# Kernel tuning notes

Hardware: AMD Instinct MI355X
Metric: run time of the kernel (lower is better)

Reference implementation:

```python
import jax, jax.numpy as jnp
import numpy as np

SHIFT = 10  # matches init kwarg shift=10


def _best_shift(x, y):
    """Per-sample argmax-Pearson shift. x, y: [B, T] -> s_best: [B] int.

    For shift s, the original pairs (x[i], y[i+s]) for all valid i
    (sf<0: x[-sf:], y[:sf]; sf>0: x[:-sf], y[sf:]).
    We realize this with a clipped gather + validity mask and compute a
    masked Pearson correlation for all 2*SHIFT+1 shifts at once.
    """
    B, T = x.shape
    shifts = jnp.arange(-SHIFT, SHIFT + 1)               # [S]
    idx = jnp.arange(T)[None, :] + shifts[:, None]        # [S, T]
    valid = (idx >= 0) & (idx < T)                        # [S, T]
    idx_c = jnp.clip(idx, 0, T - 1)
    ys = y[:, idx_c]                                      # [B, S, T] shifted y
    v = valid[None].astype(x.dtype)                       # [1, S, T]
    n = v.sum(-1)                                         # [1, S] = T - |s|
    mx = (x[:, None, :] * v).sum(-1) / n                  # [B, S]
    my = (ys * v).sum(-1) / n                             # [B, S]
    dx = (x[:, None, :] - mx[..., None]) * v              # centered, masked
    dy = (ys - my[..., None]) * v
    cov = (dx * dy).sum(-1)
    corr = cov / jnp.sqrt((dx * dx).sum(-1) * (dy * dy).sum(-1))  # [B, S]
    return shifts[jnp.argmax(corr, axis=-1)]              # [B] (first max, like torch)


def _masked_mse(x, y, s_best):
    """fn = MSE (mean reduction) over the best-shift overlap, per sample."""
    B, T = x.shape
    idx = jnp.arange(T)[None, :] + s_best[:, None]        # [B, T]
    valid = (idx >= 0) & (idx < T)
    yb = jnp.take_along_axis(y, jnp.clip(idx, 0, T - 1), axis=1)
    vf = valid.astype(x.dtype)
    d = (x - yb) * vf
    return (d * d).sum(-1) / vf.sum(-1)                   # [B]


def setup_inputs() -> dict:
    key = jax.random.key(0)
    k1, k2 = jax.random.split(key)
    B, T = 2048, 4096
    x = jax.random.normal(k1, (B, T), dtype=jnp.float32)
    # make y a noisy shifted copy of x so the shift search is meaningful
    y = jnp.roll(x, 3, axis=1) + 0.1 * jax.random.normal(k2, (B, T), dtype=jnp.float32)
    return {"x": x, "y": y}


def reference(x, y):
    s_best = _best_shift(x, y)             # [B], int (no grad path)
    return jnp.mean(_masked_mse(x, y, s_best))
```

## Files before the change

kernel.cpp:

```cpp
#include <hip/hip_runtime.h>

#define TLEN 4096
#define NQ (TLEN / 4)
#define NSHIFT 21
#define SHIFT 10
#define NTHR 256

__global__ __launch_bounds__(NTHR, 4)
void shift_corr_kernel(const float* __restrict__ x, const float* __restrict__ y,
                       float* __restrict__ mse_out)
{
    __shared__ float redbuf[4][32];

    const int tid  = threadIdx.x;
    const int row  = blockIdx.x;
    const int lane = tid & 63;
    const int wid  = tid >> 6;

    const float* xrow = x + (size_t)row * TLEN;
    const float* yrow = y + (size_t)row * TLEN;
    const float4* xg = (const float4*)xrow;
    const float4* yq = (const float4*)yrow;

    float4 xq[4];
    #pragma unroll
    for (int it = 0; it < 4; ++it)
        xq[it] = xg[tid + it * NTHR];

    float sxy[NSHIFT];
    #pragma unroll
    for (int k = 0; k < NSHIFT; ++k) sxy[k] = 0.f;
    float sx = 0.f, sxx = 0.f, sy = 0.f, syy = 0.f;

    #pragma unroll
    for (int it = 0; it < 4; ++it) {
        const int c = tid + it * NTHR;
        float xv[4] = {xq[it].x, xq[it].y, xq[it].z, xq[it].w};
        float yw[28];
        #pragma unroll
        for (int k = 0; k < 7; ++k) {
            int qi = c + k - 3;
            int qc = qi < 0 ? 0 : (qi > NQ - 1 ? NQ - 1 : qi);
            float msk = (qi == qc) ? 1.f : 0.f;
            float4 v = yq[qc];
            yw[4*k+0] = v.x * msk; yw[4*k+1] = v.y * msk;
            yw[4*k+2] = v.z * msk; yw[4*k+3] = v.w * msk;
        }
        #pragma unroll
        for (int l = 0; l < 4; ++l) {
            float xl = xv[l];
            sx += xl; sxx = fmaf(xl, xl, sxx);
            float yl = yw[12 + l];
            sy += yl; syy = fmaf(yl, yl, syy);
            #pragma unroll
            for (int si = 0; si < NSHIFT; ++si)
                sxy[si] = fmaf(xl, yw[l + si + 2], sxy[si]);
        }
    }

    float vals[32];
    #pragma unroll
    for (int k = 0; k < NSHIFT; ++k) vals[k] = sxy[k];
    vals[21] = sx; vals[22] = sxx; vals[23] = sy; vals[24] = syy;
    #pragma unroll
    for (int k = NSHIFT + 4; k < 32; ++k) vals[k] = 0.f;

    #pragma unroll
    for (int b = 5; b >= 1; --b) {
        const int mask = 1 << b;
        const int half = 1 << (b - 1);
        const bool keepLow = ((lane >> b) & 1) == 0;
        #pragma unroll
        for (int j = 0; j < half; ++j) {
            float send = keepLow ? vals[j + half] : vals[j];
            float recv = __shfl_xor(send, mask, 64);
            vals[j] = (keepLow ? vals[j] : vals[j + half]) + recv;
        }
    }
    {
        float recv = __shfl_xor(vals[0], 1, 64);
        float tot = vals[0] + recv;
        if ((lane & 1) == 0) redbuf[wid][(lane >> 1) & 31] = tot;
    }
    __syncthreads();

    if (wid == 0) {
        const int v = lane & 31;
        float S = redbuf[0][v] + redbuf[1][v] + redbuf[2][v] + redbuf[3][v];
        float Sx  = __shfl(S, 21, 64);
        float Sxx = __shfl(S, 22, 64);
        float Sy  = __shfl(S, 23, 64);
        float Syy = __shfl(S, 24, 64);

        float corr = -1e30f, mse = 0.f;
        int bsi = lane;
        if (lane < NSHIFT) {
            const int s = lane - SHIFT;
            const int k = s < 0 ? -s : s;
            float ax = 0.f, axx = 0.f, ay = 0.f, ayy = 0.f;
            if (s >= 0) {
                for (int j = 0; j < k; ++j) {
                    float xv = xrow[TLEN - 1 - j];
                    float yv = yrow[j];
                    ax += xv; axx = fmaf(xv, xv, axx);
                    ay += yv; ayy = fmaf(yv, yv, ayy);
                }
            } else {
                for (int j = 0; j < k; ++j) {
                    float xv = xrow[j];
                    float yv = yrow[TLEN - 1 - j];
                    ax += xv; axx = fmaf(xv, xv, axx);
                    ay += yv; ayy = fmaf(yv, yv, ayy);
                }
            }
            const float n = (float)(TLEN - k);
            float Sxs = Sx - ax, Sxxs = Sxx - axx;
            float Sys = Sy - ay, Syys = Syy - ayy;
            float Sxys = S;
            float cov = Sxys - Sxs * Sys / n;
            float vx  = Sxxs - Sxs * Sxs / n;
            float vy  = Syys - Sys * Sys / n;
            corr = cov * rsqrtf(vx * vy);
            mse  = (Sxxs + Syys - 2.f * Sxys) / n;
        }
        #pragma unroll
        for (int m = 32; m >= 1; m >>= 1) {
            float oc = __shfl_xor(corr, m, 64);
            float om = __shfl_xor(mse,  m, 64);
            int  osi = __shfl_xor(bsi,  m, 64);
            if (oc > corr || (oc == corr && osi < bsi)) {
                corr = oc; mse = om; bsi = osi;
            }
        }
        if (lane == 0) mse_out[row] = mse;
    }
}

__global__ __launch_bounds__(NTHR)
void finalize_kernel(const float* __restrict__ mse, float* __restrict__ out, int B)
{
    __shared__ float red[4];
    int tid = threadIdx.x;
    int lane = tid & 63, wid = tid >> 6;
    const float4* m4 = (const float4*)mse;
    float a = 0.f;
    for (int i = tid; i < B / 4; i += NTHR) {
        float4 v = m4[i];
        a += (v.x + v.y) + (v.z + v.w);
    }
    #pragma unroll
    for (int off = 32; off > 0; off >>= 1)
        a += __shfl_down(a, off, 64);
    if (lane == 0) red[wid] = a;
    __syncthreads();
    if (tid == 0) out[0] = (red[0] + red[1] + red[2] + red[3]) / (float)B;
}

extern "C" void kernel_launch(void* const* d_in, const int* in_sizes, int n_in,
                              void* d_out, int out_size, void* d_ws, size_t ws_size,
                              hipStream_t stream)
{
    const float* x = (const float*)d_in[0];
    const float* y = (const float*)d_in[1];
    float* out = (float*)d_out;
    float* ws  = (float*)d_ws;
    const int B = in_sizes[0] / TLEN;

    shift_corr_kernel<<<B, NTHR, 0, stream>>>(x, y, ws);
    finalize_kernel<<<1, NTHR, 0, stream>>>(ws, out, B);
}
```

Before: 96.36 us.

## Split each row across four blocks and add a separate Pearson kernel

The single per-row kernel is split in two. The first kernel launches four blocks per row, each processing one quarter of the row, and writes partial sums for 21 shifts plus the x and y moments to the workspace. A second kernel of one wave per row combines the partials, applies the edge corrections and selects the best shift. This raises grid parallelism and lowers per-thread registers, at the cost of an extra kernel launch, a workspace round trip, and re-reading the y halo at quarter boundaries.

```diff
diff --git a/kernel.cpp b/kernel.cpp
--- a/kernel.cpp
+++ b/kernel.cpp
@@ -5,27 +5,38 @@
 #define NSHIFT 21
 #define SHIFT 10
 #define NTHR 256
+#define PARTS 4
+#define NVAL 32
 
 __global__ __launch_bounds__(NTHR, 4)
-void shift_corr_kernel(const float* __restrict__ x, const float* __restrict__ y,
-                       float* __restrict__ mse_out)
+void partial_kernel(const float* __restrict__ x, const float* __restrict__ y,
+                    float* __restrict__ partial)
 {
-    __shared__ float redbuf[4][32];
+    __shared__ float redbuf[4][NVAL];
 
     const int tid  = threadIdx.x;
-    const int row  = blockIdx.x;
+    const int row  = blockIdx.x >> 2;
+    const int part = blockIdx.x & 3;
     const int lane = tid & 63;
     const int wid  = tid >> 6;
 
-    const float* xrow = x + (size_t)row * TLEN;
-    const float* yrow = y + (size_t)row * TLEN;
-    const float4* xg = (const float4*)xrow;
-    const float4* yq = (const float4*)yrow;
+    const float4* xg = (const float4*)(x + (size_t)row * TLEN);
+    const float4* yq = (const float4*)(y + (size_t)row * TLEN);
+    const int c = part * NTHR + tid;
 
-    float4 xq[4];
+    float4 xv4 = xg[c];
+    float xv[4] = {xv4.x, xv4.y, xv4.z, xv4.w};
+
+    float yw[28];
     #pragma unroll
-    for (int it = 0; it < 4; ++it)
-        xq[it] = xg[tid + it * NTHR];
+    for (int k = 0; k < 7; ++k) {
+        int qi = c + k - 3;
+        int qc = qi < 0 ? 0 : (qi > NQ - 1 ? NQ - 1 : qi);
+        float msk = (qi == qc) ? 1.f : 0.f;
+        float4 v = yq[qc];
+        yw[4*k+0] = v.x * msk; yw[4*k+1] = v.y * msk;
+        yw[4*k+2] = v.z * msk; yw[4*k+3] = v.w * msk;
+    }
 
     float sxy[NSHIFT];
     #pragma unroll
@@ -33,29 +44,14 @@
     float sx = 0.f, sxx = 0.f, sy = 0.f, syy = 0.f;
 
     #pragma unroll
-    for (int it = 0; it < 4; ++it) {
-        const int c = tid + it * NTHR;
-        float xv[4] = {xq[it].x, xq[it].y, xq[it].z, xq[it].w};
-        float yw[28];
+    for (int l = 0; l < 4; ++l) {
+        float xl = xv[l];
+        sx += xl; sxx = fmaf(xl, xl, sxx);
+        float yl = yw[12 + l];
+        sy += yl; syy = fmaf(yl, yl, syy);
         #pragma unroll
-        for (int k = 0; k < 7; ++k) {
-            int qi = c + k - 3;
-            int qc = qi < 0 ? 0 : (qi > NQ - 1 ? NQ - 1 : qi);
-            float msk = (qi == qc) ? 1.f : 0.f;
-            float4 v = yq[qc];
-            yw[4*k+0] = v.x * msk; yw[4*k+1] = v.y * msk;
-            yw[4*k+2] = v.z * msk; yw[4*k+3] = v.w * msk;
-        }
-        #pragma unroll
-        for (int l = 0; l < 4; ++l) {
-            float xl = xv[l];
-            sx += xl; sxx = fmaf(xl, xl, sxx);
-            float yl = yw[12 + l];
-            sy += yl; syy = fmaf(yl, yl, syy);
-            #pragma unroll
-            for (int si = 0; si < NSHIFT; ++si)
-                sxy[si] = fmaf(xl, yw[l + si + 2], sxy[si]);
-        }
+        for (int si = 0; si < NSHIFT; ++si)
+            sxy[si] = fmaf(xl, yw[l + si + 2], sxy[si]);
     }
 
     float vals[32];
@@ -84,56 +80,74 @@
     }
     __syncthreads();
 
-    if (wid == 0) {
-        const int v = lane & 31;
-        float S = redbuf[0][v] + redbuf[1][v] + redbuf[2][v] + redbuf[3][v];
-        float Sx  = __shfl(S, 21, 64);
-        float Sxx = __shfl(S, 22, 64);
-        float Sy  = __shfl(S, 23, 64);
-        float Syy = __shfl(S, 24, 64);
+    if (wid == 0 && lane < 32) {
+        float S = redbuf[0][lane] + redbuf[1][lane] + redbuf[2][lane] + redbuf[3][lane];
+        partial[(size_t)blockIdx.x * NVAL + lane] = S;
+    }
+}
 
-        float corr = -1e30f, mse = 0.f;
-        int bsi = lane;
-        if (lane < NSHIFT) {
-            const int s = lane - SHIFT;
-            const int k = s < 0 ? -s : s;
-            float ax = 0.f, axx = 0.f, ay = 0.f, ayy = 0.f;
-            if (s >= 0) {
-                for (int j = 0; j < k; ++j) {
-                    float xv = xrow[TLEN - 1 - j];
-                    float yv = yrow[j];
-                    ax += xv; axx = fmaf(xv, xv, axx);
-                    ay += yv; ayy = fmaf(yv, yv, ayy);
-                }
-            } else {
-                for (int j = 0; j < k; ++j) {
-                    float xv = xrow[j];
-                    float yv = yrow[TLEN - 1 - j];
-                    ax += xv; axx = fmaf(xv, xv, axx);
-                    ay += yv; ayy = fmaf(yv, yv, ayy);
-                }
+__global__ __launch_bounds__(64)
+void pearson_kernel(const float* __restrict__ x, const float* __restrict__ y,
+                    const float* __restrict__ partial, float* __restrict__ mse_out)
+{
+    const int row  = blockIdx.x;
+    const int lane = threadIdx.x;
+    const int v = lane & 31;
+
+    const float* xrow = x + (size_t)row * TLEN;
+    const float* yrow = y + (size_t)row * TLEN;
+
+    float S = 0.f;
+    #pragma unroll
+    for (int p = 0; p < PARTS; ++p)
+        S += partial[(size_t)(row * PARTS + p) * NVAL + v];
+
+    float Sx  = __shfl(S, 21, 64);
+    float Sxx = __shfl(S, 22, 64);
+    float Sy  = __shfl(S, 23, 64);
+    float Syy = __shfl(S, 24, 64);
+
+    float corr = -1e30f, mse = 0.f;
+    int bsi = lane;
+    if (lane < NSHIFT) {
+        const int s = lane - SHIFT;
+        const int k = s < 0 ? -s : s;
+        float ax = 0.f, axx = 0.f, ay = 0.f, ayy = 0.f;
+        if (s >= 0) {
+            for (int j = 0; j < k; ++j) {
+                float xv = xrow[TLEN - 1 - j];
+                float yv = yrow[j];
+                ax += xv; axx = fmaf(xv, xv, axx);
+                ay += yv; ayy = fmaf(yv, yv, ayy);
             }
-            const float n = (float)(TLEN - k);
-            float Sxs = Sx - ax, Sxxs = Sxx - axx;
-            float Sys = Sy - ay, Syys = Syy - ayy;
-            float Sxys = S;
-            float cov = Sxys - Sxs * Sys / n;
-            float vx  = Sxxs - Sxs * Sxs / n;
-            float vy  = Syys - Sys * Sys / n;
-            corr = cov * rsqrtf(vx * vy);
-            mse  = (Sxxs + Syys - 2.f * Sxys) / n;
-        }
-        #pragma unroll
-        for (int m = 32; m >= 1; m >>= 1) {
-            float oc = __shfl_xor(corr, m, 64);
-            float om = __shfl_xor(mse,  m, 64);
-            int  osi = __shfl_xor(bsi,  m, 64);
-            if (oc > corr || (oc == corr && osi < bsi)) {
-                corr = oc; mse = om; bsi = osi;
+        } else {
+            for (int j = 0; j < k; ++j) {
+                float xv = xrow[j];
+                float yv = yrow[TLEN - 1 - j];
+                ax += xv; axx = fmaf(xv, xv, axx);
+                ay += yv; ayy = fmaf(yv, yv, ayy);
             }
         }
-        if (lane == 0) mse_out[row] = mse;
+        const float n = (float)(TLEN - k);
+        float Sxs = Sx - ax, Sxxs = Sxx - axx;
+        float Sys = Sy - ay, Syys = Syy - ayy;
+        float Sxys = S;
+        float cov = Sxys - Sxs * Sys / n;
+        float vx  = Sxxs - Sxs * Sxs / n;
+        float vy  = Syys - Sys * Sys / n;
+        corr = cov * rsqrtf(vx * vy);
+        mse  = (Sxxs + Syys - 2.f * Sxys) / n;
     }
+    #pragma unroll
+    for (int m = 32; m >= 1; m >>= 1) {
+        float oc = __shfl_xor(corr, m, 64);
+        float om = __shfl_xor(mse,  m, 64);
+        int  osi = __shfl_xor(bsi,  m, 64);
+        if (oc > corr || (oc == corr && osi < bsi)) {
+            corr = oc; mse = om; bsi = osi;
+        }
+    }
+    if (lane == 0) mse_out[row] = mse;
 }
 
 __global__ __launch_bounds__(NTHR)
@@ -163,9 +177,12 @@
     const float* x = (const float*)d_in[0];
     const float* y = (const float*)d_in[1];
     float* out = (float*)d_out;
-    float* ws  = (float*)d_ws;
     const int B = in_sizes[0] / TLEN;
 
-    shift_corr_kernel<<<B, NTHR, 0, stream>>>(x, y, ws);
-    finalize_kernel<<<1, NTHR, 0, stream>>>(ws, out, B);
+    float* partial = (float*)d_ws;
+    float* mse     = partial + (size_t)B * PARTS * NVAL;
+
+    partial_kernel<<<B * PARTS, NTHR, 0, stream>>>(x, y, partial);
+    pearson_kernel<<<B, 64, 0, stream>>>(x, y, partial, mse);
+    finalize_kernel<<<1, NTHR, 0, stream>>>(mse, out, B);
 }
```

Result: slower. 268.1 us (+178.3%).
